# Kernel optimization log

Hardware: AMD Instinct MI355X
Metric: run time of the kernel (lower is better)

## Reference

```python
import jax, jax.numpy as jnp
import numpy as np

NUM_HEADS = 16  # config.num_attention_heads


def setup_inputs() -> dict:
    key = jax.random.key(0)
    k0, k1, k2 = jax.random.split(key, 3)
    B, S, D = 2, 2048, 2048
    hd = D // NUM_HEADS  # 128
    hidden_states = jax.random.normal(k0, (B, S, D), dtype=jnp.float32)
    c_attn_w = jax.random.normal(k1, (D + 2 * hd, D), dtype=jnp.float32) * 0.02
    c_attn_b = jnp.zeros((D + 2 * hd,), dtype=jnp.float32)
    c_proj_w = jax.random.normal(k2, (D, D), dtype=jnp.float32) * 0.02
    c_proj_b = jnp.zeros((D,), dtype=jnp.float32)
    return {
        "hidden_states": hidden_states,
        "c_attn_w": c_attn_w,
        "c_attn_b": c_attn_b,
        "c_proj_w": c_proj_w,
        "c_proj_b": c_proj_b,
    }


def reference(hidden_states, c_attn_w, c_attn_b, c_proj_w, c_proj_b):
    B, S, D = hidden_states.shape
    H = NUM_HEADS
    hd = D // H
    scale = hd ** -0.5

    # fused QKV projection: [B,S,D] -> [B,S,D+2*hd]
    qkv = hidden_states @ c_attn_w.T + c_attn_b
    # multi-query split: per-head Q, single shared K and V
    q = qkv[..., :D].reshape(B, S, H, hd)        # [B,S,H,hd]
    k = qkv[..., D:D + hd]                       # [B,S,hd]
    v = qkv[..., D + hd:]                        # [B,S,hd]

    # attention scores (full matrix materialized, like the baddbmm path)
    scores = jnp.einsum('bqhd,bkd->bhqk', q, k) * scale  # [B,H,S,S]
    causal = jnp.tril(jnp.ones((S, S), dtype=bool))
    scores = jnp.where(causal, scores, jnp.finfo(scores.dtype).min)
    attn = jax.nn.softmax(scores, axis=-1)

    # context: shared V broadcast across heads
    ctx = jnp.einsum('bhqk,bkd->bqhd', attn, v).reshape(B, S, D)
    out = ctx @ c_proj_w.T + c_proj_b
    return out
```

## Files before the change

kernel.cpp:

```cpp
#include <hip/hip_runtime.h>
#include <hip/hip_bf16.h>
#include <math.h>

typedef unsigned short u16;
typedef __attribute__((ext_vector_type(8))) __bf16 bf16x8;
typedef __attribute__((ext_vector_type(4))) float f32x4;

__device__ inline u16 f2bf(float f) {
  union { float f; unsigned u; } x; x.f = f;
  unsigned r = x.u + 0x7fffu + ((x.u >> 16) & 1u);
  return (u16)(r >> 16);
}

__device__ inline unsigned cvtpk(float lo, float hi) {
  unsigned r;
  asm("v_cvt_pk_bf16_f32 %0, %1, %2" : "=v"(r) : "v"(lo), "v"(hi));
  return r;
}

__device__ inline float fexp2(float x) {
  float r;
  asm("v_exp_f32 %0, %1" : "=v"(r) : "v"(x));
  return r;
}

__device__ inline void async16(const void* g, void* l) {
  __builtin_amdgcn_global_load_lds(
      (const __attribute__((address_space(1))) void*)g,
      (__attribute__((address_space(3))) void*)l, 16, 0, 0);
}

__global__ __launch_bounds__(256) void cast_bf16_kernel(
    const float* __restrict__ in, u16* __restrict__ out, int n4) {
  int i = blockIdx.x * 256 + threadIdx.x;
  if (i >= n4) return;
  float4 v = ((const float4*)in)[i];
  u16 o0 = f2bf(v.x), o1 = f2bf(v.y), o2 = f2bf(v.z), o3 = f2bf(v.w);
  unsigned lo = (unsigned)o0 | ((unsigned)o1 << 16);
  unsigned hi = (unsigned)o2 | ((unsigned)o3 << 16);
  ((uint2*)out)[i] = make_uint2(lo, hi);
}

__global__ __launch_bounds__(256) void vt_kernel(
    const u16* __restrict__ qkv, u16* __restrict__ vt) {
  __shared__ u16 tile[32][136];
  const int t = threadIdx.x;
  const int b = blockIdx.x >> 6;
  const int S0 = (blockIdx.x & 63) * 32;
  const int s_l = t >> 3, dg = t & 7;
  const u16* src = qkv + ((size_t)b * 2048 + S0 + s_l) * 2304 + 2176 + dg * 16;
  *(uint4*)&tile[s_l][dg * 16] = *(const uint4*)src;
  *(uint4*)&tile[s_l][dg * 16 + 8] = *(const uint4*)(src + 8);
  __syncthreads();
  const int d = t >> 1, sh = t & 1;
  u16 buf[16];
#pragma unroll
  for (int j = 0; j < 16; ++j) buf[j] = tile[sh * 16 + j][d];
  u16* dst = vt + ((size_t)b * 128 + d) * 2048 + S0 + sh * 16;
  *(uint4*)dst = *(uint4*)&buf[0];
  *(uint4*)(dst + 8) = *(uint4*)&buf[8];
}

template <bool BF16OUT>
__global__ __launch_bounds__(256) void gemm_bt(
    const u16* __restrict__ A, const u16* __restrict__ Bw,
    const float* __restrict__ bias, void* __restrict__ Cout,
    int M, int N, int K, int qcols, float qscale) {
  __shared__ u16 As[2][128 * 64];
  __shared__ u16 Bs[2][128 * 64];
  const int t = threadIdx.x;
  const int w = t >> 6;
  const int lane = t & 63;
  const int lq = lane >> 4, lr = lane & 15;

  int bx = blockIdx.x, by = blockIdx.y;
  const int gx = gridDim.x, gy = gridDim.y;
  if ((gx & 1) == 0 && (gy & 3) == 0) {
    const int cw = gx >> 1, ch = gy >> 2;
    int id = by * gx + bx;
    int xcd = id & 7, j = id >> 3;
    bx = (xcd & 1) * cw + j % cw;
    by = (xcd >> 1) * ch + j / cw;
  }

  const long brow = (long)by * 128;
  const long bcol = (long)bx * 128;
  const int wr = (w >> 1) * 64, wc = (w & 1) * 64;
  f32x4 acc[4][4] = {};

  int rA[4], cA[4];
#pragma unroll
  for (int it = 0; it < 4; ++it) {
    int ci = it * 256 + t;
    rA[it] = ci >> 3;
    cA[it] = (ci & 7) ^ (rA[it] & 7);
  }

  char* const AsB = (char*)&As[0][0];
  char* const BsB = (char*)&Bs[0][0];

  auto stage = [&](int buf, int kt) {
    char* ad = AsB + buf * 16384;
    char* bd = BsB + buf * 16384;
#pragma unroll
    for (int it = 0; it < 4; ++it) {
      const u16* srcA = A + (brow + rA[it]) * (long)K + kt + cA[it] * 8;
      async16(srcA, ad + (it * 256 + w * 64) * 16);
      const u16* srcB = Bw + (bcol + rA[it]) * (long)K + kt + cA[it] * 8;
      async16(srcB, bd + (it * 256 + w * 64) * 16);
    }
  };

  stage(0, 0);
  __syncthreads();

  int cur = 0;
  for (int kt = 0; kt < K; kt += 64) {
    if (kt + 64 < K) stage(cur ^ 1, kt + 64);
    const char* Ab = AsB + cur * 16384;
    const char* Bb = BsB + cur * 16384;
#pragma unroll
    for (int kb = 0; kb < 2; ++kb) {
      bf16x8 af[4], bfr[4];
#pragma unroll
      for (int m = 0; m < 4; ++m) {
        int row = wr + m * 16 + lr;
        int byte = (row * 128 + kb * 64 + lq * 16) ^ ((row & 7) << 4);
        af[m] = *(const bf16x8*)(Ab + byte);
      }
#pragma unroll
      for (int n = 0; n < 4; ++n) {
        int row = wc + n * 16 + lr;
        int byte = (row * 128 + kb * 64 + lq * 16) ^ ((row & 7) << 4);
        bfr[n] = *(const bf16x8*)(Bb + byte);
      }
#pragma unroll
      for (int m = 0; m < 4; ++m)
#pragma unroll
        for (int n = 0; n < 4; ++n)
          acc[m][n] = __builtin_amdgcn_mfma_f32_16x16x32_bf16(
              af[m], bfr[n], acc[m][n], 0, 0, 0);
    }
    __syncthreads();
    cur ^= 1;
  }

#pragma unroll
  for (int m = 0; m < 4; ++m) {
    long row0 = brow + wr + m * 16 + lq * 4;
#pragma unroll
    for (int n = 0; n < 4; ++n) {
      long col = bcol + wc + n * 16 + lr;
      float bv = bias[col];
      float cs = (col < qcols) ? qscale : 1.f;
#pragma unroll
      for (int j = 0; j < 4; ++j) {
        float v = (acc[m][n][j] + bv) * cs;
        if (BF16OUT)
          ((u16*)Cout)[(row0 + j) * N + col] = f2bf(v);
        else
          ((float*)Cout)[(row0 + j) * N + col] = v;
      }
    }
  }
}

__global__ __launch_bounds__(256, 2) void attn_kernel(
    const u16* __restrict__ qkv, const u16* __restrict__ vt,
    u16* __restrict__ ctx) {
  __shared__ u16 Kl[2][64 * 136];
  __shared__ u16 Vl[2][128 * 72];
  __shared__ u16 Pl[4][16 * 72];

  const int t = threadIdx.x;
  const int w = t >> 6;
  const int lane = t & 63;
  const int lq = lane >> 4, lr = lane & 15;
  const int lkey = lq * 4;
  const int bid = blockIdx.x;
  const int qtid = bid >> 5;
  const int qt = (qtid < 8) ? (15 - qtid) : (qtid - 8);
  const int hb = bid & 31;
  const int h = hb & 15;
  const int b = hb >> 4;
  const int s0w = qt * 128 + w * 32;
  const size_t qb = (size_t)b * 2048 * 2304;

  bf16x8 qg[2][4];
#pragma unroll
  for (int s = 0; s < 2; ++s)
#pragma unroll
    for (int kc = 0; kc < 4; ++kc)
      qg[s][kc] = *(const bf16x8*)(qkv + qb +
                                   (size_t)(s0w + s * 16 + lr) * 2304 +
                                   h * 128 + kc * 32 + lq * 8);

  const u16* kp[5];
  const u16* vp[5];
#pragma unroll
  for (int ii = 0; ii < 5; ++ii) {
    int I = 4 * ii + w;
    {
      int pp = I * 1024 + lane * 16;
      int row = pp / 272;
      int rem = pp - row * 272;
      int ch = (rem < 256) ? (rem >> 4) : 0;
      if (row > 63) row = 63;
      kp[ii] = qkv + qb + (size_t)row * 2304 + 2048 + ch * 8;
    }
    {
      int pp = I * 1024 + lane * 16;
      int row = pp / 144;
      int rem = pp - row * 144;
      int ch = (rem < 128) ? (rem >> 4) : 0;
      if (row > 127) row = 127;
      vp[ii] = vt + ((size_t)b * 128 + row) * 2048 + ch * 8;
    }
  }
  char* const KlB = (char*)&Kl[0][0];
  char* const VlB = (char*)&Vl[0][0];

  auto stage = [&](int buf) {
    char* kd = KlB + buf * 17408;
    char* vd = VlB + buf * 18432;
#pragma unroll
    for (int ii = 0; ii < 5; ++ii) {
      int I = 4 * ii + w;
      if (I < 17) {
        async16(kp[ii], kd + I * 1024);
        kp[ii] += 64 * 2304;
      }
    }
#pragma unroll
    for (int ii = 0; ii < 5; ++ii) {
      int I = 4 * ii + w;
      if (I < 18) {
        async16(vp[ii], vd + I * 1024);
        vp[ii] += 64;
      }
    }
  };

  const int loK = lr * 272 + lq * 16;
  const int loV = lr * 144 + lq * 16;
  char* const pb = (char*)&Pl[w][0];
  char* const pw0 = pb + lr * 144 + lq * 8;
  const char* const PL = pb + lr * 144 + lq * 16;

  float mreg[2] = {-INFINITY, -INFINITY};
  float lreg[2] = {0.f, 0.f};
  f32x4 o[2][8] = {};
  const int ntiles = 2 * qt + 2;

  stage(0);
  __syncthreads();

  int cur = 0;
  for (int j2 = 0; j2 < ntiles; ++j2) {
    const int kvb = j2 * 64;
    if (j2 + 1 < ntiles) stage(cur ^ 1);
    if (kvb <= s0w + 31) {
      const char* KL = KlB + cur * 17408 + loK;
      const char* VL = VlB + cur * 18432 + loV;
      const bool maskT = (kvb + 63 > s0w);

      f32x4 sc[2][4] = {};
#pragma unroll
      for (int g = 0; g < 4; ++g)
#pragma unroll
        for (int kc = 0; kc < 4; ++kc) {
          bf16x8 kf = *(const bf16x8*)(KL + g * 4352 + kc * 64);
          sc[0][g] = __builtin_amdgcn_mfma_f32_16x16x32_bf16(kf, qg[0][kc],
                                                             sc[0][g], 0, 0, 0);
          sc[1][g] = __builtin_amdgcn_mfma_f32_16x16x32_bf16(kf, qg[1][kc],
                                                             sc[1][g], 0, 0, 0);
        }

      bf16x8 pa[2][2];
#pragma unroll
      for (int s = 0; s < 2; ++s) {
        float vv[16];
#pragma unroll
        for (int u = 0; u < 16; ++u) vv[u] = sc[s][u >> 2][u & 3];
        if (maskT) {
          const int qrel = s0w + s * 16 + lr - kvb;
#pragma unroll
          for (int g = 0; g < 4; ++g)
#pragma unroll
            for (int r = 0; r < 4; ++r)
              if (g * 16 + lkey + r > qrel) vv[g * 4 + r] = -INFINITY;
        }
        float mx = vv[0];
#pragma unroll
        for (int u = 1; u < 16; ++u) mx = fmaxf(mx, vv[u]);
        mx = fmaxf(mx, __shfl_xor(mx, 16));
        mx = fmaxf(mx, __shfl_xor(mx, 32));
        float mn = mreg[s];
        if (__any(mx > mn + 8.f)) {
          float mu = fmaxf(mn, mx);
          float alpha = fexp2(mn - mu);
          mreg[s] = mu;
          mn = mu;
          lreg[s] *= alpha;
          float a0 = __shfl(alpha, lkey + 0);
          float a1 = __shfl(alpha, lkey + 1);
          float a2 = __shfl(alpha, lkey + 2);
          float a3 = __shfl(alpha, lkey + 3);
#pragma unroll
          for (int n = 0; n < 8; ++n) {
            o[s][n][0] *= a0;
            o[s][n][1] *= a1;
            o[s][n][2] *= a2;
            o[s][n][3] *= a3;
          }
        }
        float rs = 0.f;
#pragma unroll
        for (int g = 0; g < 4; ++g)
#pragma unroll
          for (int rp = 0; rp < 2; ++rp) {
            float p0 = fexp2(vv[g * 4 + 2 * rp] - mn);
            float p1 = fexp2(vv[g * 4 + 2 * rp + 1] - mn);
            rs += p0 + p1;
            *(unsigned*)(pw0 + g * 32 + rp * 4) = cvtpk(p0, p1);
          }
        rs += __shfl_xor(rs, 16);
        rs += __shfl_xor(rs, 32);
        lreg[s] += rs;
        pa[s][0] = *(const bf16x8*)(PL);
        pa[s][1] = *(const bf16x8*)(PL + 64);
      }

#pragma unroll
      for (int n = 0; n < 8; ++n) {
        bf16x8 vf0 = *(const bf16x8*)(VL + n * 2304);
        bf16x8 vf1 = *(const bf16x8*)(VL + n * 2304 + 64);
        o[0][n] = __builtin_amdgcn_mfma_f32_16x16x32_bf16(pa[0][0], vf0,
                                                          o[0][n], 0, 0, 0);
        o[0][n] = __builtin_amdgcn_mfma_f32_16x16x32_bf16(pa[0][1], vf1,
                                                          o[0][n], 0, 0, 0);
        o[1][n] = __builtin_amdgcn_mfma_f32_16x16x32_bf16(pa[1][0], vf0,
                                                          o[1][n], 0, 0, 0);
        o[1][n] = __builtin_amdgcn_mfma_f32_16x16x32_bf16(pa[1][1], vf1,
                                                          o[1][n], 0, 0, 0);
      }
    }
    __syncthreads();
    cur ^= 1;
  }

#pragma unroll
  for (int s = 0; s < 2; ++s) {
    float inv = 1.f / lreg[s];
    float iv[4];
    iv[0] = __shfl(inv, lkey + 0);
    iv[1] = __shfl(inv, lkey + 1);
    iv[2] = __shfl(inv, lkey + 2);
    iv[3] = __shfl(inv, lkey + 3);
#pragma unroll
    for (int r = 0; r < 4; ++r) {
      size_t rowoff =
          ((size_t)b * 2048 + s0w + s * 16 + lkey + r) * 2048 + h * 128;
#pragma unroll
      for (int n = 0; n < 8; ++n)
        ctx[rowoff + n * 16 + lr] = f2bf(o[s][n][r] * iv[r]);
    }
  }
}

extern "C" void kernel_launch(void* const* d_in, const int* in_sizes, int n_in,
                              void* d_out, int out_size, void* d_ws,
                              size_t ws_size, hipStream_t stream) {
  (void)in_sizes; (void)n_in; (void)out_size; (void)ws_size;
  const float* hs = (const float*)d_in[0];
  const float* attn_w = (const float*)d_in[1];
  const float* attn_b = (const float*)d_in[2];
  const float* proj_w = (const float*)d_in[3];
  const float* proj_b = (const float*)d_in[4];
  float* out = (float*)d_out;

  u16* hs_b = (u16*)d_ws;
  u16* aw_b = hs_b + (size_t)4096 * 2048;
  u16* pw_b = aw_b + (size_t)2304 * 2048;
  u16* qkv_b = pw_b + (size_t)2048 * 2048;
  u16* vt_b = qkv_b + (size_t)4096 * 2304;
  u16* ctx_b = vt_b + (size_t)2 * 128 * 2048;

  const float qscale = 0.08838834764831845f * 1.4426950408889634f;

  cast_bf16_kernel<<<8192, 256, 0, stream>>>(hs, hs_b, 2097152);
  cast_bf16_kernel<<<4608, 256, 0, stream>>>(attn_w, aw_b, 1179648);
  cast_bf16_kernel<<<4096, 256, 0, stream>>>(proj_w, pw_b, 1048576);

  gemm_bt<true><<<dim3(18, 32), 256, 0, stream>>>(hs_b, aw_b, attn_b, qkv_b,
                                                  4096, 2304, 2048, 2048,
                                                  qscale);
  vt_kernel<<<128, 256, 0, stream>>>(qkv_b, vt_b);
  attn_kernel<<<512, 256, 0, stream>>>(qkv_b, vt_b, ctx_b);
  gemm_bt<false><<<dim3(16, 32), 256, 0, stream>>>(ctx_b, pw_b, proj_b, out,
                                                   4096, 2048, 2048, 0, 1.f);
}
```

Measured before the change: 195.4 us.

## Triple-buffer GEMM with K-tile 32 and fine-grained vmcnt waits

```diff
diff --git a/kernel.cpp b/kernel.cpp
--- a/kernel.cpp
+++ b/kernel.cpp
@@ -62,12 +62,11 @@
 }
 
 template <bool BF16OUT>
-__global__ __launch_bounds__(256) void gemm_bt(
+__global__ __launch_bounds__(256, 4) void gemm_bt(
     const u16* __restrict__ A, const u16* __restrict__ Bw,
     const float* __restrict__ bias, void* __restrict__ Cout,
     int M, int N, int K, int qcols, float qscale) {
-  __shared__ u16 As[2][128 * 64];
-  __shared__ u16 Bs[2][128 * 64];
+  __shared__ u16 Ls[3][2][128 * 32];
   const int t = threadIdx.x;
   const int w = t >> 6;
   const int lane = t & 63;
@@ -88,61 +87,69 @@
   const int wr = (w >> 1) * 64, wc = (w & 1) * 64;
   f32x4 acc[4][4] = {};
 
-  int rA[4], cA[4];
-#pragma unroll
-  for (int it = 0; it < 4; ++it) {
+  const u16* pA[2];
+  const u16* pB[2];
+#pragma unroll
+  for (int it = 0; it < 2; ++it) {
     int ci = it * 256 + t;
-    rA[it] = ci >> 3;
-    cA[it] = (ci & 7) ^ (rA[it] & 7);
-  }
-
-  char* const AsB = (char*)&As[0][0];
-  char* const BsB = (char*)&Bs[0][0];
-
-  auto stage = [&](int buf, int kt) {
-    char* ad = AsB + buf * 16384;
-    char* bd = BsB + buf * 16384;
-#pragma unroll
-    for (int it = 0; it < 4; ++it) {
-      const u16* srcA = A + (brow + rA[it]) * (long)K + kt + cA[it] * 8;
-      async16(srcA, ad + (it * 256 + w * 64) * 16);
-      const u16* srcB = Bw + (bcol + rA[it]) * (long)K + kt + cA[it] * 8;
-      async16(srcB, bd + (it * 256 + w * 64) * 16);
+    int row = ci >> 2;
+    int ch = (ci & 3) ^ (row & 3);
+    pA[it] = A + (brow + row) * (long)K + ch * 8;
+    pB[it] = Bw + (bcol + row) * (long)K + ch * 8;
+  }
+
+  char* const L = (char*)&Ls[0][0][0];
+  auto stageTo = [&](int off) {
+#pragma unroll
+    for (int it = 0; it < 2; ++it) {
+      async16(pA[it], L + off + (it * 256 + w * 64) * 16);
+      pA[it] += 32;
+    }
+#pragma unroll
+    for (int it = 0; it < 2; ++it) {
+      async16(pB[it], L + off + 8192 + (it * 256 + w * 64) * 16);
+      pB[it] += 32;
     }
   };
 
-  stage(0, 0);
-  __syncthreads();
-
-  int cur = 0;
-  for (int kt = 0; kt < K; kt += 64) {
-    if (kt + 64 < K) stage(cur ^ 1, kt + 64);
-    const char* Ab = AsB + cur * 16384;
-    const char* Bb = BsB + cur * 16384;
-#pragma unroll
-    for (int kb = 0; kb < 2; ++kb) {
-      bf16x8 af[4], bfr[4];
-#pragma unroll
-      for (int m = 0; m < 4; ++m) {
-        int row = wr + m * 16 + lr;
-        int byte = (row * 128 + kb * 64 + lq * 16) ^ ((row & 7) << 4);
-        af[m] = *(const bf16x8*)(Ab + byte);
-      }
-#pragma unroll
-      for (int n = 0; n < 4; ++n) {
-        int row = wc + n * 16 + lr;
-        int byte = (row * 128 + kb * 64 + lq * 16) ^ ((row & 7) << 4);
-        bfr[n] = *(const bf16x8*)(Bb + byte);
-      }
-#pragma unroll
-      for (int m = 0; m < 4; ++m)
-#pragma unroll
-        for (int n = 0; n < 4; ++n)
-          acc[m][n] = __builtin_amdgcn_mfma_f32_16x16x32_bf16(
-              af[m], bfr[n], acc[m][n], 0, 0, 0);
-    }
-    __syncthreads();
-    cur ^= 1;
+  const int aBase = (wr + lr) * 64 + ((lq ^ (lr & 3)) << 4);
+  const int bBase = 8192 + (wc + lr) * 64 + ((lq ^ (lr & 3)) << 4);
+
+  auto computeFrom = [&](int off) {
+    const char* Ab = L + off + aBase;
+    const char* Bb = L + off + bBase;
+    bf16x8 af[4], bfr[4];
+#pragma unroll
+    for (int m = 0; m < 4; ++m) af[m] = *(const bf16x8*)(Ab + m * 1024);
+#pragma unroll
+    for (int n = 0; n < 4; ++n) bfr[n] = *(const bf16x8*)(Bb + n * 1024);
+#pragma unroll
+    for (int m = 0; m < 4; ++m)
+#pragma unroll
+      for (int n = 0; n < 4; ++n)
+        acc[m][n] = __builtin_amdgcn_mfma_f32_16x16x32_bf16(
+            af[m], bfr[n], acc[m][n], 0, 0, 0);
+  };
+
+  stageTo(0);
+  stageTo(16384);
+  asm volatile("s_waitcnt vmcnt(4)" ::: "memory");
+  __builtin_amdgcn_s_barrier();
+
+  int oc = 0, osg = 32768;
+  for (int kt = 0; kt < K; kt += 32) {
+    if (kt + 64 < K) {
+      stageTo(osg);
+      computeFrom(oc);
+      asm volatile("s_waitcnt vmcnt(4) lgkmcnt(0)" ::: "memory");
+    } else {
+      computeFrom(oc);
+      asm volatile("s_waitcnt vmcnt(0) lgkmcnt(0)" ::: "memory");
+    }
+    __builtin_amdgcn_s_barrier();
+    osg = oc;
+    oc += 16384;
+    if (oc == 49152) oc = 0;
   }
 
 #pragma unroll
```

New measurement: 229.1 us. 1.17x slower.

## Load V fragments directly from global memory instead of staging through LDS

Applied to the files above, without the earlier changes.

```diff
diff --git a/kernel.cpp b/kernel.cpp
--- a/kernel.cpp
+++ b/kernel.cpp
@@ -165,11 +165,10 @@
   }
 }
 
-__global__ __launch_bounds__(256, 2) void attn_kernel(
+__global__ __launch_bounds__(256, 3) void attn_kernel(
     const u16* __restrict__ qkv, const u16* __restrict__ vt,
     u16* __restrict__ ctx) {
   __shared__ u16 Kl[2][64 * 136];
-  __shared__ u16 Vl[2][128 * 72];
   __shared__ u16 Pl[4][16 * 72];
 
   const int t = threadIdx.x;
@@ -196,33 +195,20 @@
                                    h * 128 + kc * 32 + lq * 8);
 
   const u16* kp[5];
-  const u16* vp[5];
 #pragma unroll
   for (int ii = 0; ii < 5; ++ii) {
     int I = 4 * ii + w;
-    {
-      int pp = I * 1024 + lane * 16;
-      int row = pp / 272;
-      int rem = pp - row * 272;
-      int ch = (rem < 256) ? (rem >> 4) : 0;
-      if (row > 63) row = 63;
-      kp[ii] = qkv + qb + (size_t)row * 2304 + 2048 + ch * 8;
-    }
-    {
-      int pp = I * 1024 + lane * 16;
-      int row = pp / 144;
-      int rem = pp - row * 144;
-      int ch = (rem < 128) ? (rem >> 4) : 0;
-      if (row > 127) row = 127;
-      vp[ii] = vt + ((size_t)b * 128 + row) * 2048 + ch * 8;
-    }
+    int pp = I * 1024 + lane * 16;
+    int row = pp / 272;
+    int rem = pp - row * 272;
+    int ch = (rem < 256) ? (rem >> 4) : 0;
+    if (row > 63) row = 63;
+    kp[ii] = qkv + qb + (size_t)row * 2304 + 2048 + ch * 8;
   }
   char* const KlB = (char*)&Kl[0][0];
-  char* const VlB = (char*)&Vl[0][0];
 
   auto stage = [&](int buf) {
     char* kd = KlB + buf * 17408;
-    char* vd = VlB + buf * 18432;
 #pragma unroll
     for (int ii = 0; ii < 5; ++ii) {
       int I = 4 * ii + w;
@@ -231,21 +217,13 @@
         kp[ii] += 64 * 2304;
       }
     }
-#pragma unroll
-    for (int ii = 0; ii < 5; ++ii) {
-      int I = 4 * ii + w;
-      if (I < 18) {
-        async16(vp[ii], vd + I * 1024);
-        vp[ii] += 64;
-      }
-    }
   };
 
   const int loK = lr * 272 + lq * 16;
-  const int loV = lr * 144 + lq * 16;
   char* const pb = (char*)&Pl[w][0];
   char* const pw0 = pb + lr * 144 + lq * 8;
   const char* const PL = pb + lr * 144 + lq * 16;
+  const u16* const vroot = vt + ((size_t)b * 128 + lr) * 2048 + lq * 8;
 
   float mreg[2] = {-INFINITY, -INFINITY};
   float lreg[2] = {0.f, 0.f};
@@ -261,7 +239,6 @@
     if (j2 + 1 < ntiles) stage(cur ^ 1);
     if (kvb <= s0w + 31) {
       const char* KL = KlB + cur * 17408 + loK;
-      const char* VL = VlB + cur * 18432 + loV;
       const bool maskT = (kvb + 63 > s0w);
 
       f32x4 sc[2][4] = {};
@@ -331,10 +308,11 @@
         pa[s][1] = *(const bf16x8*)(PL + 64);
       }
 
+      const u16* vg = vroot + kvb;
 #pragma unroll
       for (int n = 0; n < 8; ++n) {
-        bf16x8 vf0 = *(const bf16x8*)(VL + n * 2304);
-        bf16x8 vf1 = *(const bf16x8*)(VL + n * 2304 + 64);
+        bf16x8 vf0 = *(const bf16x8*)(vg + (size_t)n * 16 * 2048);
+        bf16x8 vf1 = *(const bf16x8*)(vg + (size_t)n * 16 * 2048 + 32);
         o[0][n] = __builtin_amdgcn_mfma_f32_16x16x32_bf16(pa[0][0], vf0,
                                                           o[0][n], 0, 0, 0);
         o[0][n] = __builtin_amdgcn_mfma_f32_16x16x32_bf16(pa[0][1], vf1,
```

New measurement: 272.9 us. 1.4x slower.
